# Kernel tuning notes

Hardware: AMD Instinct MI355X
Metric: run time of the kernel (lower is better)

## Reference

```python
import jax, jax.numpy as jnp
import numpy as np

N = 20000      # nodes
E = 640000     # edges
IN = 2         # in_dim
H = 4          # heads
C = 64         # hidden_dim (per-head channels)
ED = 3         # edge_dim
K = 4          # num_clusters
EPS = 1e-16    # PyG softmax eps


def setup_inputs():
    key = jax.random.key(0)
    ks = jax.random.split(key, 32)
    g = lambda i, sh: (jax.random.normal(ks[i], sh, dtype=jnp.float32) * 0.1)
    inp = {
        'x': jax.random.normal(ks[0], (N, IN), dtype=jnp.float32),
        'edge_index': jax.random.randint(ks[1], (2, E), 0, N, dtype=jnp.int64),
        'edge_attr': jax.random.normal(ks[2], (E, ED), dtype=jnp.float32),
        # input_proj
        'Wp': g(3, (IN, C)), 'bp': g(4, (C,)),
        # conv1: in C -> H*C, concat
        'W1': g(5, (C, H * C)), 'We1': g(6, (ED, H * C)),
        'as1': g(7, (H, C)), 'ad1': g(8, (H, C)), 'ae1': g(9, (H, C)), 'b1': g(10, (H * C,)),
        # conv2: in H*C -> H*C, concat
        'W2': g(11, (H * C, H * C)), 'We2': g(12, (ED, H * C)),
        'as2': g(13, (H, C)), 'ad2': g(14, (H, C)), 'ae2': g(15, (H, C)), 'b2': g(16, (H * C,)),
        # conv3: in H*C -> C, heads=1
        'W3': g(17, (H * C, C)), 'We3': g(18, (ED, C)),
        'as3': g(19, (1, C)), 'ad3': g(20, (1, C)), 'ae3': g(21, (1, C)), 'b3': g(22, (C,)),
        # classifier
        'Wc': g(23, (C, K)), 'bc': g(24, (K,)),
    }
    return inp


def _gat(h, src, dst, edge_attr, W, We, a_src, a_dst, a_edge, bias, heads, cph):
    """PyG GATConv (shared lin for src/dst, edge_dim, concat=True), eval mode."""
    xh = (h @ W).reshape(N, heads, cph)                       # [N,H,C]
    alpha_src = jnp.einsum('nhc,hc->nh', xh, a_src)           # [N,H]
    alpha_dst = jnp.einsum('nhc,hc->nh', xh, a_dst)
    eh = (edge_attr @ We).reshape(E, heads, cph)              # [E,H,C]
    alpha = alpha_src[src] + alpha_dst[dst] + jnp.einsum('ehc,hc->eh', eh, a_edge)
    alpha = jax.nn.leaky_relu(alpha, 0.2)                     # [E,H]
    # segment softmax over destination neighborhoods
    m = jax.ops.segment_max(alpha, dst, num_segments=N)       # [N,H]
    ea = jnp.exp(alpha - m[dst])
    s = jax.ops.segment_sum(ea, dst, num_segments=N)
    attn = ea / (s[dst] + EPS)                                # [E,H]
    msg = xh[src] * attn[:, :, None]                          # [E,H,C]
    out = jax.ops.segment_sum(msg, dst, num_segments=N)       # [N,H,C]
    return out.reshape(N, heads * cph) + bias


def reference(x, edge_index, edge_attr, Wp, bp,
              W1, We1, as1, ad1, ae1, b1,
              W2, We2, as2, ad2, ae2, b2,
              W3, We3, as3, ad3, ae3, b3,
              Wc, bc):
    src, dst = edge_index[0], edge_index[1]
    h = jax.nn.elu(x @ Wp + bp)
    h = jax.nn.elu(_gat(h, src, dst, edge_attr, W1, We1, as1, ad1, ae1, b1, H, C))
    h = jax.nn.elu(_gat(h, src, dst, edge_attr, W2, We2, as2, ad2, ae2, b2, H, C))
    h = _gat(h, src, dst, edge_attr, W3, We3, as3, ad3, ae3, b3, 1, C)
    return jax.nn.softmax(h @ Wc + bc, axis=-1)
```

## Files before the change

### kernel.cpp

```cpp
#include <hip/hip_runtime.h>
#include <math.h>

#define N_NODES 20000
#define N_EDGES 640000

typedef __attribute__((ext_vector_type(8))) short short8;
typedef __attribute__((ext_vector_type(4))) float floatx4;

__device__ __forceinline__ float elu_f(float v) { return v > 0.f ? v : expm1f(v); }

__device__ __forceinline__ unsigned short bf16_rne(float f) {
  union { float f; unsigned u; } v;
  v.f = f;
  unsigned r = v.u + 0x7FFF + ((v.u >> 16) & 1);
  return (unsigned short)(r >> 16);
}

__device__ __forceinline__ float bf_to_f(unsigned short u) {
  union { unsigned u; float f; } v;
  v.u = (unsigned)u << 16;
  return v.f;
}


__global__ void zero_int_kernel(int* p, int n) {
  int i = blockIdx.x * 256 + threadIdx.x;
  if (i < n) p[i] = 0;
}

__global__ void hist_kernel(const int* __restrict__ dst, int* __restrict__ cnt, int ne) {
  int e = blockIdx.x * 256 + threadIdx.x;
  if (e < ne) atomicAdd(&cnt[dst[e]], 1);
}

__global__ __launch_bounds__(1024) void scan_kernel(const int* __restrict__ cnt,
                                                    int* __restrict__ row_ptr,
                                                    int* __restrict__ row_next, int n) {
  __shared__ int part[1024];
  int t = threadIdx.x;
  int per = (n + 1023) / 1024;
  int base = t * per;
  int local = 0;
  for (int i = 0; i < per; ++i) {
    int idx = base + i;
    if (idx < n) local += cnt[idx];
  }
  part[t] = local;
  __syncthreads();
  for (int off = 1; off < 1024; off <<= 1) {
    int v = (t >= off) ? part[t - off] : 0;
    __syncthreads();
    part[t] += v;
    __syncthreads();
  }
  int prefix = (t == 0) ? 0 : part[t - 1];
  for (int i = 0; i < per; ++i) {
    int idx = base + i;
    if (idx < n) {
      row_ptr[idx] = prefix;
      row_next[idx] = prefix;
      prefix += cnt[idx];
    }
  }
  if (t == 1023) row_ptr[n] = part[1023];
}

__global__ void fill_kernel(const int* __restrict__ dst, int* __restrict__ row_next,
                            int* __restrict__ csr_eid, int ne) {
  int e = blockIdx.x * 256 + threadIdx.x;
  if (e >= ne) return;
  int pos = atomicAdd(&row_next[dst[e]], 1);
  csr_eid[pos] = e;
}


__global__ void wt_all_kernel(const float* __restrict__ W1, const float* __restrict__ W2,
                              const float* __restrict__ W3, unsigned short* __restrict__ Bt1,
                              unsigned short* __restrict__ Bt2, unsigned short* __restrict__ Bt3) {
  int idx = blockIdx.x * 256 + threadIdx.x;
  const float* W; unsigned short* Bt; int K, Nc, local;
  if (idx < 16384)      { W = W1; Bt = Bt1; K = 64;  Nc = 256; local = idx; }
  else if (idx < 81920) { W = W2; Bt = Bt2; K = 256; Nc = 256; local = idx - 16384; }
  else if (idx < 98304) { W = W3; Bt = Bt3; K = 256; Nc = 64;  local = idx - 81920; }
  else return;
  int k = local / Nc, n = local - k * Nc;
  Bt[(size_t)n * K + k] = bf16_rne(W[local]);
}


__global__ void aeproj_all_kernel(const float* __restrict__ We1, const float* __restrict__ ae1,
                                  const float* __restrict__ We2, const float* __restrict__ ae2,
                                  const float* __restrict__ We3, const float* __restrict__ ae3,
                                  float* __restrict__ proj) {
  int t = threadIdx.x;
  if (t < 12) {
    int d = t >> 2, h = t & 3;
    float s = 0.f;
    for (int c = 0; c < 64; ++c) s += We1[d * 256 + h * 64 + c] * ae1[h * 64 + c];
    proj[t] = s;
  } else if (t < 24) {
    int u = t - 12; int d = u >> 2, h = u & 3;
    float s = 0.f;
    for (int c = 0; c < 64; ++c) s += We2[d * 256 + h * 64 + c] * ae2[h * 64 + c];
    proj[t] = s;
  } else if (t < 27) {
    int d = t - 24;
    float s = 0.f;
    for (int c = 0; c < 64; ++c) s += We3[d * 64 + c] * ae3[c];
    proj[t] = s;
  }
}


__global__ void in_proj_kernel(const float* __restrict__ x, const float* __restrict__ Wp,
                               const float* __restrict__ bp, unsigned short* __restrict__ h_bf,
                               int n) {
  int i = blockIdx.x * 256 + threadIdx.x;
  if (i >= n * 64) return;
  int node = i >> 6, c = i & 63;
  float v = x[node * 2] * Wp[c] + x[node * 2 + 1] * Wp[64 + c] + bp[c];
  h_bf[i] = bf16_rne(elu_f(v));
}


template <int KDIM>
__global__ __launch_bounds__(256) void mfma_gemm_alpha_kernel(
    const unsigned short* __restrict__ A, const unsigned short* __restrict__ Bt,
    unsigned short* __restrict__ C_bf, const float* __restrict__ a_src,
    const float* __restrict__ a_dst, float* __restrict__ alp_s,
    float* __restrict__ alp_d, int M, int Nc) {
  __shared__ unsigned short As[64][40];
  __shared__ unsigned short Bs[64][40];
  int t = threadIdx.x;
  int wave = t >> 6, lane = t & 63;
  int m_frag = lane & 15, quad = lane >> 4;
  int row0 = blockIdx.y * 64, col0 = blockIdx.x * 64;
  int lr = t >> 2;
  int lk = (t & 3) * 8;
  floatx4 acc[4];
  #pragma unroll
  for (int c = 0; c < 4; ++c) acc[c] = (floatx4){0.f, 0.f, 0.f, 0.f};

  for (int k0 = 0; k0 < KDIM; k0 += 32) {
    int gr = row0 + lr;
    short8 av = {0, 0, 0, 0, 0, 0, 0, 0};
    if (gr < M) av = *(const short8*)(A + (size_t)gr * KDIM + k0 + lk);
    *(short8*)(&As[lr][lk]) = av;
    short8 bv = *(const short8*)(Bt + (size_t)(col0 + lr) * KDIM + k0 + lk);
    *(short8*)(&Bs[lr][lk]) = bv;
    __syncthreads();
    short8 a = *(const short8*)(&As[wave * 16 + m_frag][quad * 8]);
    #pragma unroll
    for (int c = 0; c < 4; ++c) {
      short8 b = *(const short8*)(&Bs[c * 16 + m_frag][quad * 8]);
      acc[c] = __builtin_amdgcn_mfma_f32_16x16x32_bf16(a, b, acc[c], 0, 0, 0);
    }
    __syncthreads();
  }

  int H = Nc >> 6;
  int head = blockIdx.x;
  float ps[4] = {}, pd[4] = {};
  #pragma unroll
  for (int c = 0; c < 4; ++c) {
    float asv = a_src[head * 64 + c * 16 + m_frag];
    float adv = a_dst[head * 64 + c * 16 + m_frag];
    #pragma unroll
    for (int i = 0; i < 4; ++i) {
      ps[i] += acc[c][i] * asv;
      pd[i] += acc[c][i] * adv;
    }
  }
  #pragma unroll
  for (int off = 1; off < 16; off <<= 1) {
    #pragma unroll
    for (int i = 0; i < 4; ++i) {
      ps[i] += __shfl_xor(ps[i], off);
      pd[i] += __shfl_xor(pd[i], off);
    }
  }
  #pragma unroll
  for (int c = 0; c < 4; ++c) {
    #pragma unroll
    for (int i = 0; i < 4; ++i) {
      int gr = row0 + wave * 16 + quad * 4 + i;
      if (gr < M) C_bf[(size_t)gr * Nc + col0 + c * 16 + m_frag] = bf16_rne(acc[c][i]);
    }
  }
  if (m_frag == 0) {
    #pragma unroll
    for (int i = 0; i < 4; ++i) {
      int gr = row0 + wave * 16 + quad * 4 + i;
      if (gr < M) {
        alp_s[gr * H + head] = ps[i];
        alp_d[gr * H + head] = pd[i];
      }
    }
  }
}


template <int HC, bool APPLY_ELU, bool OUT_BF>
__global__ __launch_bounds__(256) void softagg_kernel(
    const int* __restrict__ row_ptr, const int* __restrict__ csr_eid,
    const int* __restrict__ src_arr, const float* __restrict__ ea,
    const float* __restrict__ alp_s, const float* __restrict__ alp_d,
    const float* __restrict__ proj, const unsigned short* __restrict__ xh_bf,
    const float* __restrict__ bias, float* __restrict__ out,
    unsigned short* __restrict__ out_bf) {
  constexpr int H = HC / 64;
  constexpr int CHUNK = 256;
  constexpr int L = HC / 8;
  constexpr int S = 256 / L;
  __shared__ float lds_w[H][CHUNK];
  __shared__ int lds_src[CHUNK];
  __shared__ float sh_r[H];
  __shared__ float sh_inv[H];
  __shared__ float red[S * HC];

  int n = blockIdx.x;
  int t = threadIdx.x;
  int wave = t >> 6, lane = t & 63;
  int slot = t / L, l = t % L;
  int head2 = (8 * l) >> 6;
  int s0 = row_ptr[n], s1 = row_ptr[n + 1];

  float m_run = -INFINITY, s_run = 0.f;
  float acc[8] = {};
  float adv = 0.f, p0 = 0.f, p1 = 0.f, p2 = 0.f;
  if (wave < H) {
    adv = alp_d[n * H + wave];
    p0 = proj[0 * H + wave];
    p1 = proj[1 * H + wave];
    p2 = proj[2 * H + wave];
  }

  for (int c0 = s0; c0 < s1; c0 += CHUNK) {
    int cend = min(s1, c0 + CHUNK);
    if (wave < H) {
      int h = wave;
      float cm = -INFINITY;
      for (int i = c0 + lane; i < cend; i += 64) {
        int eid = csr_eid[i];
        int s = src_arr[eid];
        if (h == 0) lds_src[i - c0] = s;
        float a = alp_s[s * H + h] + adv
                + ea[eid * 3 + 0] * p0 + ea[eid * 3 + 1] * p1 + ea[eid * 3 + 2] * p2;
        a = a > 0.f ? a : 0.2f * a;
        lds_w[h][i - c0] = a;
        cm = fmaxf(cm, a);
      }
      #pragma unroll
      for (int off = 1; off < 64; off <<= 1) cm = fmaxf(cm, __shfl_xor(cm, off));
      float m_new = fmaxf(m_run, cm);
      float r = __expf(m_run - m_new);
      float se = 0.f;
      for (int i = c0 + lane; i < cend; i += 64) {
        float w = __expf(lds_w[h][i - c0] - m_new);
        lds_w[h][i - c0] = w;
        se += w;
      }
      #pragma unroll
      for (int off = 1; off < 64; off <<= 1) se += __shfl_xor(se, off);
      s_run = s_run * r + se;
      m_run = m_new;
      if (lane == 0) sh_r[h] = r;
    }
    __syncthreads();
    float rr = sh_r[head2];
    #pragma unroll
    for (int j = 0; j < 8; ++j) acc[j] *= rr;
    for (int i = c0 + slot; i < cend; i += S) {
      float w = lds_w[head2][i - c0];
      int s = lds_src[i - c0];
      short8 v = *(const short8*)(xh_bf + (size_t)s * HC + l * 8);
      #pragma unroll
      for (int j = 0; j < 8; ++j) acc[j] += bf_to_f((unsigned short)v[j]) * w;
    }
    __syncthreads();
  }
  if (wave < H && lane == 0) sh_inv[wave] = 1.0f / (s_run + 1e-16f);
  __syncthreads();
  float inv = sh_inv[head2];
  #pragma unroll
  for (int j = 0; j < 8; ++j) red[slot * HC + l * 8 + j] = acc[j] * inv;
  __syncthreads();
  if (t < HC) {
    float a = 0.f;
    #pragma unroll
    for (int s = 0; s < S; ++s) a += red[s * HC + t];
    a += bias[t];
    if (APPLY_ELU) a = elu_f(a);
    if (OUT_BF) out_bf[(size_t)n * HC + t] = bf16_rne(a);
    else out[(size_t)n * HC + t] = a;
  }
}


__global__ void classifier_kernel(const float* __restrict__ h, const float* __restrict__ Wc,
                                  const float* __restrict__ bc, float* __restrict__ out,
                                  int n_nodes) {
  int gid = blockIdx.x * 256 + threadIdx.x;
  int w = gid >> 6, lane = gid & 63;
  if (w >= n_nodes) return;
  float hv = h[w * 64 + lane];
  float p0 = hv * Wc[lane * 4 + 0];
  float p1 = hv * Wc[lane * 4 + 1];
  float p2 = hv * Wc[lane * 4 + 2];
  float p3 = hv * Wc[lane * 4 + 3];
  for (int off = 32; off; off >>= 1) {
    p0 += __shfl_down(p0, off);
    p1 += __shfl_down(p1, off);
    p2 += __shfl_down(p2, off);
    p3 += __shfl_down(p3, off);
  }
  if (lane == 0) {
    p0 += bc[0]; p1 += bc[1]; p2 += bc[2]; p3 += bc[3];
    float mx = fmaxf(fmaxf(p0, p1), fmaxf(p2, p3));
    float e0 = __expf(p0 - mx), e1 = __expf(p1 - mx), e2 = __expf(p2 - mx), e3 = __expf(p3 - mx);
    float inv = 1.f / (e0 + e1 + e2 + e3);
    out[w * 4 + 0] = e0 * inv;
    out[w * 4 + 1] = e1 * inv;
    out[w * 4 + 2] = e2 * inv;
    out[w * 4 + 3] = e3 * inv;
  }
}


extern "C" void kernel_launch(void* const* d_in, const int* in_sizes, int n_in,
                              void* d_out, int out_size, void* d_ws, size_t ws_size,
                              hipStream_t stream) {
  const float* x   = (const float*)d_in[0];
  const int*   ei  = (const int*)d_in[1];
  const float* ea  = (const float*)d_in[2];
  const float* Wp  = (const float*)d_in[3];
  const float* bp  = (const float*)d_in[4];
  const float* W1  = (const float*)d_in[5];
  const float* We1 = (const float*)d_in[6];
  const float* as1 = (const float*)d_in[7];
  const float* ad1 = (const float*)d_in[8];
  const float* ae1 = (const float*)d_in[9];
  const float* b1  = (const float*)d_in[10];
  const float* W2  = (const float*)d_in[11];
  const float* We2 = (const float*)d_in[12];
  const float* as2 = (const float*)d_in[13];
  const float* ad2 = (const float*)d_in[14];
  const float* ae2 = (const float*)d_in[15];
  const float* b2  = (const float*)d_in[16];
  const float* W3  = (const float*)d_in[17];
  const float* We3 = (const float*)d_in[18];
  const float* as3 = (const float*)d_in[19];
  const float* ad3 = (const float*)d_in[20];
  const float* ae3 = (const float*)d_in[21];
  const float* b3  = (const float*)d_in[22];
  const float* Wc  = (const float*)d_in[23];
  const float* bc  = (const float*)d_in[24];
  float* out = (float*)d_out;

  const int* src = ei;
  const int* dst = ei + N_EDGES;

  char* wptr = (char*)d_ws;
  auto alloc = [&](size_t bytes) {
    char* p = wptr;
    wptr += (bytes + 255) & ~(size_t)255;
    return p;
  };
  int*            cnt      = (int*)alloc((size_t)N_NODES * 4);
  int*            row_ptr  = (int*)alloc((size_t)(N_NODES + 1) * 4);
  int*            row_next = (int*)alloc((size_t)N_NODES * 4);
  int*            csr_eid  = (int*)alloc((size_t)N_EDGES * 4);
  unsigned short* hA_bf    = (unsigned short*)alloc((size_t)N_NODES * 256 * 2);
  unsigned short* hX_bf    = (unsigned short*)alloc((size_t)N_NODES * 256 * 2);
  float*          hC       = (float*)alloc((size_t)N_NODES * 64 * 4);
  float*          alp_s    = (float*)alloc((size_t)N_NODES * 4 * 4);
  float*          alp_d    = (float*)alloc((size_t)N_NODES * 4 * 4);
  float*          proj     = (float*)alloc(32 * 4);
  unsigned short* Bt1      = (unsigned short*)alloc((size_t)64 * 256 * 2);
  unsigned short* Bt2      = (unsigned short*)alloc((size_t)256 * 256 * 2);
  unsigned short* Bt3      = (unsigned short*)alloc((size_t)256 * 64 * 2);

  zero_int_kernel<<<(N_NODES + 255) / 256, 256, 0, stream>>>(cnt, N_NODES);
  hist_kernel<<<(N_EDGES + 255) / 256, 256, 0, stream>>>(dst, cnt, N_EDGES);
  scan_kernel<<<1, 1024, 0, stream>>>(cnt, row_ptr, row_next, N_NODES);
  fill_kernel<<<(N_EDGES + 255) / 256, 256, 0, stream>>>(dst, row_next, csr_eid, N_EDGES);

  wt_all_kernel<<<(98304 + 255) / 256, 256, 0, stream>>>(W1, W2, W3, Bt1, Bt2, Bt3);
  aeproj_all_kernel<<<1, 64, 0, stream>>>(We1, ae1, We2, ae2, We3, ae3, proj);

  in_proj_kernel<<<N_NODES * 64 / 256, 256, 0, stream>>>(x, Wp, bp, hA_bf, N_NODES);

  dim3 g256(4, (N_NODES + 63) / 64);
  dim3 g64(1, (N_NODES + 63) / 64);

  mfma_gemm_alpha_kernel<64><<<g256, 256, 0, stream>>>(hA_bf, Bt1, hX_bf, as1, ad1,
                                                       alp_s, alp_d, N_NODES, 256);
  softagg_kernel<256, true, true><<<N_NODES, 256, 0, stream>>>(row_ptr, csr_eid, src, ea,
                                                               alp_s, alp_d, proj + 0, hX_bf,
                                                               b1, nullptr, hA_bf);

  mfma_gemm_alpha_kernel<256><<<g256, 256, 0, stream>>>(hA_bf, Bt2, hX_bf, as2, ad2,
                                                        alp_s, alp_d, N_NODES, 256);
  softagg_kernel<256, true, true><<<N_NODES, 256, 0, stream>>>(row_ptr, csr_eid, src, ea,
                                                               alp_s, alp_d, proj + 12, hX_bf,
                                                               b2, nullptr, hA_bf);

  mfma_gemm_alpha_kernel<256><<<g64, 256, 0, stream>>>(hA_bf, Bt3, hX_bf, as3, ad3,
                                                       alp_s, alp_d, N_NODES, 64);
  softagg_kernel<64, false, false><<<N_NODES, 256, 0, stream>>>(row_ptr, csr_eid, src, ea,
                                                                alp_s, alp_d, proj + 24, hX_bf,
                                                                b3, hC, nullptr);

  classifier_kernel<<<N_NODES * 64 / 256, 256, 0, stream>>>(hC, Wc, bc, out, N_NODES);
}
```

Before: 423.2 us.

## Reorder layer-1 GAT to aggregate 64-dim inputs before projecting, fold attention vectors

Uses linearity to aggregate the 64-channel input features per head first and apply W1 afterwards in a GEMM with fused bias and ELU. The per-edge gather shrinks from 256 bf16 channels to 64. The attention logits for layer 1 come from precomputed W1·a vectors inside the input projection kernel. The softagg reductions now use wave shuffles plus a small swizzled LDS buffer instead of a full slot-by-channel LDS reduction. The cost is an extra intermediate, slightly different bf16 rounding order, and heavier per-thread accumulators (4x8 floats) in the new aggregation kernel.

```diff
diff --git a/kernel.cpp b/kernel.cpp
--- a/kernel.cpp
+++ b/kernel.cpp
@@ -20,6 +20,10 @@
   union { unsigned u; float f; } v;
   v.u = (unsigned)u << 16;
   return v.f;
+}
+
+__device__ __forceinline__ int swz(int c) {
+  return (c & ~7) | ((((c & 7) + ((c >> 3) >> 2))) & 7);
 }
 
 
@@ -88,38 +92,67 @@
 }
 
 
-__global__ void aeproj_all_kernel(const float* __restrict__ We1, const float* __restrict__ ae1,
-                                  const float* __restrict__ We2, const float* __restrict__ ae2,
-                                  const float* __restrict__ We3, const float* __restrict__ ae3,
-                                  float* __restrict__ proj) {
+__global__ void prep_kernel(const float* __restrict__ W1, const float* __restrict__ as1,
+                            const float* __restrict__ ad1, const float* __restrict__ We1,
+                            const float* __restrict__ ae1, const float* __restrict__ We2,
+                            const float* __restrict__ ae2, const float* __restrict__ We3,
+                            const float* __restrict__ ae3, float* __restrict__ u_s,
+                            float* __restrict__ u_d, float* __restrict__ proj) {
   int t = threadIdx.x;
-  if (t < 12) {
-    int d = t >> 2, h = t & 3;
+  if (t < 256) {
+    int h = t >> 6, k = t & 63;
+    float ss = 0.f, sd = 0.f;
+    for (int c = 0; c < 64; ++c) {
+      float w = W1[k * 256 + h * 64 + c];
+      ss += w * as1[h * 64 + c];
+      sd += w * ad1[h * 64 + c];
+    }
+    u_s[t] = ss;
+    u_d[t] = sd;
+  } else if (t < 256 + 12) {
+    int u = t - 256; int d = u >> 2, h = u & 3;
     float s = 0.f;
     for (int c = 0; c < 64; ++c) s += We1[d * 256 + h * 64 + c] * ae1[h * 64 + c];
-    proj[t] = s;
-  } else if (t < 24) {
-    int u = t - 12; int d = u >> 2, h = u & 3;
+    proj[u] = s;
+  } else if (t < 256 + 24) {
+    int u = t - 256 - 12; int d = u >> 2, h = u & 3;
     float s = 0.f;
     for (int c = 0; c < 64; ++c) s += We2[d * 256 + h * 64 + c] * ae2[h * 64 + c];
-    proj[t] = s;
-  } else if (t < 27) {
-    int d = t - 24;
+    proj[12 + u] = s;
+  } else if (t < 256 + 27) {
+    int d = t - 256 - 24;
     float s = 0.f;
     for (int c = 0; c < 64; ++c) s += We3[d * 64 + c] * ae3[c];
-    proj[t] = s;
-  }
-}
-
-
-__global__ void in_proj_kernel(const float* __restrict__ x, const float* __restrict__ Wp,
-                               const float* __restrict__ bp, unsigned short* __restrict__ h_bf,
-                               int n) {
-  int i = blockIdx.x * 256 + threadIdx.x;
-  if (i >= n * 64) return;
-  int node = i >> 6, c = i & 63;
-  float v = x[node * 2] * Wp[c] + x[node * 2 + 1] * Wp[64 + c] + bp[c];
-  h_bf[i] = bf16_rne(elu_f(v));
+    proj[24 + d] = s;
+  }
+}
+
+
+__global__ void in_proj_alpha_kernel(const float* __restrict__ x, const float* __restrict__ Wp,
+                                     const float* __restrict__ bp, const float* __restrict__ u_s,
+                                     const float* __restrict__ u_d,
+                                     unsigned short* __restrict__ h_bf,
+                                     float* __restrict__ alp_s, float* __restrict__ alp_d,
+                                     int n) {
+  int gid = blockIdx.x * 256 + threadIdx.x;
+  int w = gid >> 6, lane = gid & 63;
+  if (w >= n) return;
+  float v = elu_f(x[w * 2] * Wp[lane] + x[w * 2 + 1] * Wp[64 + lane] + bp[lane]);
+  h_bf[w * 64 + lane] = bf16_rne(v);
+  #pragma unroll
+  for (int h = 0; h < 4; ++h) {
+    float ps = v * u_s[h * 64 + lane];
+    float pd = v * u_d[h * 64 + lane];
+    #pragma unroll
+    for (int off = 32; off; off >>= 1) {
+      ps += __shfl_down(ps, off);
+      pd += __shfl_down(pd, off);
+    }
+    if (lane == 0) {
+      alp_s[w * 4 + h] = ps;
+      alp_d[w * 4 + h] = pd;
+    }
+  }
 }
 
 
@@ -197,6 +230,153 @@
       }
     }
   }
+}
+
+
+__global__ __launch_bounds__(256) void mfma_gemm_be_kernel(
+    const unsigned short* __restrict__ A, const unsigned short* __restrict__ Bt,
+    const float* __restrict__ bias, unsigned short* __restrict__ C_bf, int M) {
+  __shared__ unsigned short As[64][40];
+  __shared__ unsigned short Bs[64][40];
+  int t = threadIdx.x;
+  int wave = t >> 6, lane = t & 63;
+  int m_frag = lane & 15, quad = lane >> 4;
+  int row0 = blockIdx.y * 64, col0 = blockIdx.x * 64;
+  int lr = t >> 2;
+  int lk = (t & 3) * 8;
+  floatx4 acc[4];
+  #pragma unroll
+  for (int c = 0; c < 4; ++c) acc[c] = (floatx4){0.f, 0.f, 0.f, 0.f};
+
+  for (int k0 = 0; k0 < 64; k0 += 32) {
+    int gr = row0 + lr;
+    short8 av = {0, 0, 0, 0, 0, 0, 0, 0};
+    if (gr < M) av = *(const short8*)(A + (size_t)gr * 256 + col0 + k0 + lk);
+    *(short8*)(&As[lr][lk]) = av;
+    short8 bv = *(const short8*)(Bt + (size_t)(col0 + lr) * 64 + k0 + lk);
+    *(short8*)(&Bs[lr][lk]) = bv;
+    __syncthreads();
+    short8 a = *(const short8*)(&As[wave * 16 + m_frag][quad * 8]);
+    #pragma unroll
+    for (int c = 0; c < 4; ++c) {
+      short8 b = *(const short8*)(&Bs[c * 16 + m_frag][quad * 8]);
+      acc[c] = __builtin_amdgcn_mfma_f32_16x16x32_bf16(a, b, acc[c], 0, 0, 0);
+    }
+    __syncthreads();
+  }
+  #pragma unroll
+  for (int c = 0; c < 4; ++c) {
+    float bv = bias[col0 + c * 16 + m_frag];
+    #pragma unroll
+    for (int i = 0; i < 4; ++i) {
+      int gr = row0 + wave * 16 + quad * 4 + i;
+      if (gr < M) C_bf[(size_t)gr * 256 + col0 + c * 16 + m_frag] = bf16_rne(elu_f(acc[c][i] + bv));
+    }
+  }
+}
+
+
+__global__ __launch_bounds__(256) void softagg_in_kernel(
+    const int* __restrict__ row_ptr, const int* __restrict__ csr_eid,
+    const int* __restrict__ src_arr, const float* __restrict__ ea,
+    const float* __restrict__ alp_s, const float* __restrict__ alp_d,
+    const float* __restrict__ proj, const unsigned short* __restrict__ h_bf,
+    unsigned short* __restrict__ agg_bf) {
+  constexpr int CHUNK = 256;
+  __shared__ float lds_w[4][CHUNK];
+  __shared__ int lds_src[CHUNK];
+  __shared__ float sh_r[4];
+  __shared__ float sh_inv[4];
+  __shared__ float red[4 * 256];
+
+  int n = blockIdx.x;
+  int t = threadIdx.x;
+  int wave = t >> 6, lane = t & 63;
+  int slot = t >> 3, l = t & 7;
+  int s0 = row_ptr[n], s1 = row_ptr[n + 1];
+
+  float m_run = -INFINITY, s_run = 0.f;
+  float acc[4][8] = {};
+  float adv = alp_d[n * 4 + wave];
+  float p0 = proj[0 * 4 + wave], p1 = proj[1 * 4 + wave], p2 = proj[2 * 4 + wave];
+
+  for (int c0 = s0; c0 < s1; c0 += CHUNK) {
+    int cend = min(s1, c0 + CHUNK);
+    {
+      int h = wave;
+      float cm = -INFINITY;
+      for (int i = c0 + lane; i < cend; i += 64) {
+        int eid = csr_eid[i];
+        int s = src_arr[eid];
+        if (h == 0) lds_src[i - c0] = s;
+        float a = alp_s[s * 4 + h] + adv
+                + ea[eid * 3 + 0] * p0 + ea[eid * 3 + 1] * p1 + ea[eid * 3 + 2] * p2;
+        a = a > 0.f ? a : 0.2f * a;
+        lds_w[h][i - c0] = a;
+        cm = fmaxf(cm, a);
+      }
+      #pragma unroll
+      for (int off = 1; off < 64; off <<= 1) cm = fmaxf(cm, __shfl_xor(cm, off));
+      float m_new = fmaxf(m_run, cm);
+      float r = __expf(m_run - m_new);
+      float se = 0.f;
+      for (int i = c0 + lane; i < cend; i += 64) {
+        float w = __expf(lds_w[h][i - c0] - m_new);
+        lds_w[h][i - c0] = w;
+        se += w;
+      }
+      #pragma unroll
+      for (int off = 1; off < 64; off <<= 1) se += __shfl_xor(se, off);
+      s_run = s_run * r + se;
+      m_run = m_new;
+      if (lane == 0) sh_r[h] = r;
+    }
+    __syncthreads();
+    float r0 = sh_r[0], r1 = sh_r[1], r2 = sh_r[2], r3 = sh_r[3];
+    #pragma unroll
+    for (int j = 0; j < 8; ++j) {
+      acc[0][j] *= r0; acc[1][j] *= r1; acc[2][j] *= r2; acc[3][j] *= r3;
+    }
+    for (int i = c0 + slot; i < cend; i += 32) {
+      int s = lds_src[i - c0];
+      float w0 = lds_w[0][i - c0], w1 = lds_w[1][i - c0];
+      float w2 = lds_w[2][i - c0], w3 = lds_w[3][i - c0];
+      short8 v = *(const short8*)(h_bf + (size_t)s * 64 + l * 8);
+      #pragma unroll
+      for (int j = 0; j < 8; ++j) {
+        float f = bf_to_f((unsigned short)v[j]);
+        acc[0][j] += f * w0; acc[1][j] += f * w1; acc[2][j] += f * w2; acc[3][j] += f * w3;
+      }
+    }
+    __syncthreads();
+  }
+  if (lane == 0) sh_inv[wave] = 1.0f / (s_run + 1e-16f);
+  __syncthreads();
+  float i0 = sh_inv[0], i1 = sh_inv[1], i2 = sh_inv[2], i3 = sh_inv[3];
+  #pragma unroll
+  for (int j = 0; j < 8; ++j) {
+    acc[0][j] *= i0; acc[1][j] *= i1; acc[2][j] *= i2; acc[3][j] *= i3;
+  }
+  #pragma unroll
+  for (int off = 8; off < 64; off <<= 1) {
+    #pragma unroll
+    for (int h = 0; h < 4; ++h) {
+      #pragma unroll
+      for (int j = 0; j < 8; ++j) acc[h][j] += __shfl_xor(acc[h][j], off);
+    }
+  }
+  if (lane < 8) {
+    #pragma unroll
+    for (int h = 0; h < 4; ++h) {
+      #pragma unroll
+      for (int j = 0; j < 8; ++j) red[wave * 256 + h * 64 + swz(l * 8 + j)] = acc[h][j];
+    }
+  }
+  __syncthreads();
+  int hh = t >> 6, cc = t & 63;
+  int pos = hh * 64 + swz(cc);
+  float a = red[0 * 256 + pos] + red[1 * 256 + pos] + red[2 * 256 + pos] + red[3 * 256 + pos];
+  agg_bf[(size_t)n * 256 + t] = bf16_rne(a);
 }
 
 
@@ -216,7 +396,7 @@
   __shared__ int lds_src[CHUNK];
   __shared__ float sh_r[H];
   __shared__ float sh_inv[H];
-  __shared__ float red[S * HC];
+  __shared__ float red[4 * HC];
 
   int n = blockIdx.x;
   int t = threadIdx.x;
@@ -283,12 +463,20 @@
   __syncthreads();
   float inv = sh_inv[head2];
   #pragma unroll
-  for (int j = 0; j < 8; ++j) red[slot * HC + l * 8 + j] = acc[j] * inv;
+  for (int j = 0; j < 8; ++j) acc[j] *= inv;
+  #pragma unroll
+  for (int off = L; off < 64; off <<= 1) {
+    #pragma unroll
+    for (int j = 0; j < 8; ++j) acc[j] += __shfl_xor(acc[j], off);
+  }
+  if (lane < L) {
+    #pragma unroll
+    for (int j = 0; j < 8; ++j) red[wave * HC + swz(lane * 8 + j)] = acc[j];
+  }
   __syncthreads();
   if (t < HC) {
-    float a = 0.f;
-    #pragma unroll
-    for (int s = 0; s < S; ++s) a += red[s * HC + t];
+    int pos = swz(t);
+    float a = red[0 * HC + pos] + red[1 * HC + pos] + red[2 * HC + pos] + red[3 * HC + pos];
     a += bias[t];
     if (APPLY_ELU) a = elu_f(a);
     if (OUT_BF) out_bf[(size_t)n * HC + t] = bf16_rne(a);
@@ -370,12 +558,15 @@
   int*            row_ptr  = (int*)alloc((size_t)(N_NODES + 1) * 4);
   int*            row_next = (int*)alloc((size_t)N_NODES * 4);
   int*            csr_eid  = (int*)alloc((size_t)N_EDGES * 4);
+  unsigned short* hH_bf    = (unsigned short*)alloc((size_t)N_NODES * 64 * 2);
   unsigned short* hA_bf    = (unsigned short*)alloc((size_t)N_NODES * 256 * 2);
   unsigned short* hX_bf    = (unsigned short*)alloc((size_t)N_NODES * 256 * 2);
   float*          hC       = (float*)alloc((size_t)N_NODES * 64 * 4);
   float*          alp_s    = (float*)alloc((size_t)N_NODES * 4 * 4);
   float*          alp_d    = (float*)alloc((size_t)N_NODES * 4 * 4);
   float*          proj     = (float*)alloc(32 * 4);
+  float*          u_s      = (float*)alloc(256 * 4);
+  float*          u_d      = (float*)alloc(256 * 4);
   unsigned short* Bt1      = (unsigned short*)alloc((size_t)64 * 256 * 2);
   unsigned short* Bt2      = (unsigned short*)alloc((size_t)256 * 256 * 2);
   unsigned short* Bt3      = (unsigned short*)alloc((size_t)256 * 64 * 2);
@@ -386,18 +577,17 @@
   fill_kernel<<<(N_EDGES + 255) / 256, 256, 0, stream>>>(dst, row_next, csr_eid, N_EDGES);
 
   wt_all_kernel<<<(98304 + 255) / 256, 256, 0, stream>>>(W1, W2, W3, Bt1, Bt2, Bt3);
-  aeproj_all_kernel<<<1, 64, 0, stream>>>(We1, ae1, We2, ae2, We3, ae3, proj);
-
-  in_proj_kernel<<<N_NODES * 64 / 256, 256, 0, stream>>>(x, Wp, bp, hA_bf, N_NODES);
+  prep_kernel<<<1, 512, 0, stream>>>(W1, as1, ad1, We1, ae1, We2, ae2, We3, ae3, u_s, u_d, proj);
+
+  in_proj_alpha_kernel<<<(N_NODES * 64 + 255) / 256, 256, 0, stream>>>(x, Wp, bp, u_s, u_d,
+                                                                       hH_bf, alp_s, alp_d, N_NODES);
 
   dim3 g256(4, (N_NODES + 63) / 64);
   dim3 g64(1, (N_NODES + 63) / 64);
 
-  mfma_gemm_alpha_kernel<64><<<g256, 256, 0, stream>>>(hA_bf, Bt1, hX_bf, as1, ad1,
-                                                       alp_s, alp_d, N_NODES, 256);
-  softagg_kernel<256, true, true><<<N_NODES, 256, 0, stream>>>(row_ptr, csr_eid, src, ea,
-                                                               alp_s, alp_d, proj + 0, hX_bf,
-                                                               b1, nullptr, hA_bf);
+  softagg_in_kernel<<<N_NODES, 256, 0, stream>>>(row_ptr, csr_eid, src, ea, alp_s, alp_d,
+                                                 proj + 0, hH_bf, hX_bf);
+  mfma_gemm_be_kernel<<<g256, 256, 0, stream>>>(hX_bf, Bt1, b1, hA_bf, N_NODES);
 
   mfma_gemm_alpha_kernel<256><<<g256, 256, 0, stream>>>(hA_bf, Bt2, hX_bf, as2, ad2,
                                                         alp_s, alp_d, N_NODES, 256);
```

New measurement: 495.2 us. 17.0% more time.

## Precompute CSR-ordered sources and edge attention terms, shuffle-reduce aggregation

Applied to the files above, without the earlier changes.

Adds an edge_prep kernel that writes source indices in CSR order and the per-head edge-attention dot products for all three layers once, so each softagg pass reads contiguous arrays instead of gathering through csr_eid into src and edge_attr. The aggregation loop is unrolled by two to keep more gathers in flight, and the cross-slot reduction now uses wave shuffles plus a small swizzled LDS buffer instead of a large shared array. The trade is an extra kernel and about 23MB of extra workspace traffic.

```diff
diff --git a/kernel.cpp b/kernel.cpp
--- a/kernel.cpp
+++ b/kernel.cpp
@@ -20,6 +20,10 @@
   union { unsigned u; float f; } v;
   v.u = (unsigned)u << 16;
   return v.f;
+}
+
+__device__ __forceinline__ int swz(int c) {
+  return (c & ~7) | ((((c & 7) + ((c >> 3) >> 2))) & 7);
 }
 
 
@@ -102,13 +106,31 @@
     int u = t - 12; int d = u >> 2, h = u & 3;
     float s = 0.f;
     for (int c = 0; c < 64; ++c) s += We2[d * 256 + h * 64 + c] * ae2[h * 64 + c];
-    proj[t] = s;
+    proj[12 + u] = s;
   } else if (t < 27) {
     int d = t - 24;
     float s = 0.f;
     for (int c = 0; c < 64; ++c) s += We3[d * 64 + c] * ae3[c];
-    proj[t] = s;
-  }
+    proj[24 + d] = s;
+  }
+}
+
+
+__global__ void edge_prep_kernel(const int* __restrict__ csr_eid, const int* __restrict__ src,
+                                 const float* __restrict__ ea, const float* __restrict__ proj,
+                                 int* __restrict__ csr_src, float* __restrict__ edot) {
+  int i = blockIdx.x * 256 + threadIdx.x;
+  if (i >= N_EDGES) return;
+  int eid = csr_eid[i];
+  csr_src[i] = src[eid];
+  float e0 = ea[eid * 3 + 0], e1 = ea[eid * 3 + 1], e2 = ea[eid * 3 + 2];
+  #pragma unroll
+  for (int h = 0; h < 4; ++h)
+    edot[(size_t)h * N_EDGES + i] = e0 * proj[h] + e1 * proj[4 + h] + e2 * proj[8 + h];
+  #pragma unroll
+  for (int h = 0; h < 4; ++h)
+    edot[(size_t)(4 + h) * N_EDGES + i] = e0 * proj[12 + h] + e1 * proj[16 + h] + e2 * proj[20 + h];
+  edot[(size_t)8 * N_EDGES + i] = e0 * proj[24] + e1 * proj[25] + e2 * proj[26];
 }
 
 
@@ -202,10 +224,9 @@
 
 template <int HC, bool APPLY_ELU, bool OUT_BF>
 __global__ __launch_bounds__(256) void softagg_kernel(
-    const int* __restrict__ row_ptr, const int* __restrict__ csr_eid,
-    const int* __restrict__ src_arr, const float* __restrict__ ea,
-    const float* __restrict__ alp_s, const float* __restrict__ alp_d,
-    const float* __restrict__ proj, const unsigned short* __restrict__ xh_bf,
+    const int* __restrict__ row_ptr, const int* __restrict__ csr_src,
+    const float* __restrict__ edot, const float* __restrict__ alp_s,
+    const float* __restrict__ alp_d, const unsigned short* __restrict__ xh_bf,
     const float* __restrict__ bias, float* __restrict__ out,
     unsigned short* __restrict__ out_bf) {
   constexpr int H = HC / 64;
@@ -216,7 +237,7 @@
   __shared__ int lds_src[CHUNK];
   __shared__ float sh_r[H];
   __shared__ float sh_inv[H];
-  __shared__ float red[S * HC];
+  __shared__ float red[4 * HC];
 
   int n = blockIdx.x;
   int t = threadIdx.x;
@@ -227,13 +248,9 @@
 
   float m_run = -INFINITY, s_run = 0.f;
   float acc[8] = {};
-  float adv = 0.f, p0 = 0.f, p1 = 0.f, p2 = 0.f;
-  if (wave < H) {
-    adv = alp_d[n * H + wave];
-    p0 = proj[0 * H + wave];
-    p1 = proj[1 * H + wave];
-    p2 = proj[2 * H + wave];
-  }
+  float adv = 0.f;
+  const float* __restrict__ edot_h = edot + (size_t)wave * N_EDGES;
+  if (wave < H) adv = alp_d[n * H + wave];
 
   for (int c0 = s0; c0 < s1; c0 += CHUNK) {
     int cend = min(s1, c0 + CHUNK);
@@ -241,11 +258,9 @@
       int h = wave;
       float cm = -INFINITY;
       for (int i = c0 + lane; i < cend; i += 64) {
-        int eid = csr_eid[i];
-        int s = src_arr[eid];
+        int s = csr_src[i];
         if (h == 0) lds_src[i - c0] = s;
-        float a = alp_s[s * H + h] + adv
-                + ea[eid * 3 + 0] * p0 + ea[eid * 3 + 1] * p1 + ea[eid * 3 + 2] * p2;
+        float a = alp_s[s * H + h] + adv + edot_h[i];
         a = a > 0.f ? a : 0.2f * a;
         lds_w[h][i - c0] = a;
         cm = fmaxf(cm, a);
@@ -270,9 +285,22 @@
     float rr = sh_r[head2];
     #pragma unroll
     for (int j = 0; j < 8; ++j) acc[j] *= rr;
-    for (int i = c0 + slot; i < cend; i += S) {
+    int i = c0 + slot;
+    for (; i + S < cend; i += 2 * S) {
+      int sA = lds_src[i - c0];
+      int sB = lds_src[i - c0 + S];
+      float wA = lds_w[head2][i - c0];
+      float wB = lds_w[head2][i - c0 + S];
+      short8 vA = *(const short8*)(xh_bf + (size_t)sA * HC + l * 8);
+      short8 vB = *(const short8*)(xh_bf + (size_t)sB * HC + l * 8);
+      #pragma unroll
+      for (int j = 0; j < 8; ++j) acc[j] += bf_to_f((unsigned short)vA[j]) * wA;
+      #pragma unroll
+      for (int j = 0; j < 8; ++j) acc[j] += bf_to_f((unsigned short)vB[j]) * wB;
+    }
+    if (i < cend) {
+      int s = lds_src[i - c0];
       float w = lds_w[head2][i - c0];
-      int s = lds_src[i - c0];
       short8 v = *(const short8*)(xh_bf + (size_t)s * HC + l * 8);
       #pragma unroll
       for (int j = 0; j < 8; ++j) acc[j] += bf_to_f((unsigned short)v[j]) * w;
@@ -283,12 +311,20 @@
   __syncthreads();
   float inv = sh_inv[head2];
   #pragma unroll
-  for (int j = 0; j < 8; ++j) red[slot * HC + l * 8 + j] = acc[j] * inv;
+  for (int j = 0; j < 8; ++j) acc[j] *= inv;
+  #pragma unroll
+  for (int off = L; off < 64; off <<= 1) {
+    #pragma unroll
+    for (int j = 0; j < 8; ++j) acc[j] += __shfl_xor(acc[j], off);
+  }
+  if (lane < L) {
+    #pragma unroll
+    for (int j = 0; j < 8; ++j) red[wave * HC + swz(lane * 8 + j)] = acc[j];
+  }
   __syncthreads();
   if (t < HC) {
-    float a = 0.f;
-    #pragma unroll
-    for (int s = 0; s < S; ++s) a += red[s * HC + t];
+    int pos = swz(t);
+    float a = red[0 * HC + pos] + red[1 * HC + pos] + red[2 * HC + pos] + red[3 * HC + pos];
     a += bias[t];
     if (APPLY_ELU) a = elu_f(a);
     if (OUT_BF) out_bf[(size_t)n * HC + t] = bf16_rne(a);
@@ -370,6 +406,8 @@
   int*            row_ptr  = (int*)alloc((size_t)(N_NODES + 1) * 4);
   int*            row_next = (int*)alloc((size_t)N_NODES * 4);
   int*            csr_eid  = (int*)alloc((size_t)N_EDGES * 4);
+  int*            csr_src  = (int*)alloc((size_t)N_EDGES * 4);
+  float*          edot     = (float*)alloc((size_t)9 * N_EDGES * 4);
   unsigned short* hA_bf    = (unsigned short*)alloc((size_t)N_NODES * 256 * 2);
   unsigned short* hX_bf    = (unsigned short*)alloc((size_t)N_NODES * 256 * 2);
   float*          hC       = (float*)alloc((size_t)N_NODES * 64 * 4);
@@ -387,6 +425,8 @@
 
   wt_all_kernel<<<(98304 + 255) / 256, 256, 0, stream>>>(W1, W2, W3, Bt1, Bt2, Bt3);
   aeproj_all_kernel<<<1, 64, 0, stream>>>(We1, ae1, We2, ae2, We3, ae3, proj);
+  edge_prep_kernel<<<(N_EDGES + 255) / 256, 256, 0, stream>>>(csr_eid, src, ea, proj,
+                                                              csr_src, edot);
 
   in_proj_kernel<<<N_NODES * 64 / 256, 256, 0, stream>>>(x, Wp, bp, hA_bf, N_NODES);
 
@@ -395,20 +435,23 @@
 
   mfma_gemm_alpha_kernel<64><<<g256, 256, 0, stream>>>(hA_bf, Bt1, hX_bf, as1, ad1,
                                                        alp_s, alp_d, N_NODES, 256);
-  softagg_kernel<256, true, true><<<N_NODES, 256, 0, stream>>>(row_ptr, csr_eid, src, ea,
-                                                               alp_s, alp_d, proj + 0, hX_bf,
+  softagg_kernel<256, true, true><<<N_NODES, 256, 0, stream>>>(row_ptr, csr_src,
+                                                               edot + (size_t)0 * N_EDGES,
+                                                               alp_s, alp_d, hX_bf,
                                                                b1, nullptr, hA_bf);
 
   mfma_gemm_alpha_kernel<256><<<g256, 256, 0, stream>>>(hA_bf, Bt2, hX_bf, as2, ad2,
                                                         alp_s, alp_d, N_NODES, 256);
-  softagg_kernel<256, true, true><<<N_NODES, 256, 0, stream>>>(row_ptr, csr_eid, src, ea,
-                                                               alp_s, alp_d, proj + 12, hX_bf,
+  softagg_kernel<256, true, true><<<N_NODES, 256, 0, stream>>>(row_ptr, csr_src,
+                                                               edot + (size_t)4 * N_EDGES,
+                                                               alp_s, alp_d, hX_bf,
                                                                b2, nullptr, hA_bf);
 
   mfma_gemm_alpha_kernel<256><<<g64, 256, 0, stream>>>(hA_bf, Bt3, hX_bf, as3, ad3,
                                                        alp_s, alp_d, N_NODES, 64);
-  softagg_kernel<64, false, false><<<N_NODES, 256, 0, stream>>>(row_ptr, csr_eid, src, ea,
-                                                                alp_s, alp_d, proj + 24, hX_bf,
+  softagg_kernel<64, false, false><<<N_NODES, 256, 0, stream>>>(row_ptr, csr_src,
+                                                                edot + (size_t)8 * N_EDGES,
+                                                                alp_s, alp_d, hX_bf,
                                                                 b3, hC, nullptr);
 
   classifier_kernel<<<N_NODES * 64 / 256, 256, 0, stream>>>(hC, Wc, bc, out, N_NODES);
```

Result: no change. 423.1 us (-0.0%).
